# Performance work log

Measured on AMD Instinct MI355X. Metric: run time of the kernel, lower is better.

Reference implementation:

```python
import jax, jax.numpy as jnp
import numpy as np

NEG_SLOPE = 0.2  # PyG GATConv default leaky_relu negative_slope


def gat_conv(x, edge_index, W, att_src, att_dst, bias, heads, out_ch):
    """PyG GATConv (add_self_loops=False, concat=True, dropout disabled)."""
    N = x.shape[0]
    src, dst = edge_index[0], edge_index[1]
    h = (x @ W).reshape(N, heads, out_ch)               # [N,H,C]
    a_src = jnp.einsum('nhc,hc->nh', h, att_src)        # [N,H]
    a_dst = jnp.einsum('nhc,hc->nh', h, att_dst)        # [N,H]
    e = jax.nn.leaky_relu(a_src[src] + a_dst[dst], NEG_SLOPE)  # [E,H]
    # segment softmax over edges grouped by destination node
    e_max = jax.ops.segment_max(e, dst, num_segments=N)  # [N,H]
    e_exp = jnp.exp(e - e_max[dst])
    denom = jax.ops.segment_sum(e_exp, dst, num_segments=N)
    alpha = e_exp / (denom[dst] + 1e-16)                 # [E,H]
    msg = h[src] * alpha[:, :, None]                     # [E,H,C]
    out = jax.ops.segment_sum(msg, dst, num_segments=N)  # [N,H,C]
    return out.reshape(N, heads * out_ch) + bias


def setup_inputs() -> dict:
    key = jax.random.key(0)
    ks = jax.random.split(key, 10)
    N, E, F_IN, H, C1, OUT = 50000, 1600000, 256, 8, 8, 64
    s = 0.1
    return {
        'x': jax.random.normal(ks[0], (N, F_IN), jnp.float32),
        'edge_index': jax.random.randint(ks[1], (2, E), 0, N, jnp.int64),
        'W1': jax.random.normal(ks[2], (F_IN, H * C1), jnp.float32) * s,
        'att_src1': jax.random.normal(ks[3], (H, C1), jnp.float32) * s,
        'att_dst1': jax.random.normal(ks[4], (H, C1), jnp.float32) * s,
        'bias1': jax.random.normal(ks[5], (H * C1,), jnp.float32) * s,
        'W2': jax.random.normal(ks[6], (H * C1, OUT), jnp.float32) * s,
        'att_src2': jax.random.normal(ks[7], (1, OUT), jnp.float32) * s,
        'att_dst2': jax.random.normal(ks[8], (1, OUT), jnp.float32) * s,
        'bias2': jax.random.normal(ks[9], (OUT,), jnp.float32) * s,
    }


def reference(x, edge_index, W1, att_src1, att_dst1, bias1, W2, att_src2, att_dst2, bias2):
    # GAT.forward, eval mode with disable_dropout=True (no dropout, no loss)
    h = gat_conv(x, edge_index, W1, att_src1, att_dst1, bias1, heads=8, out_ch=8)
    h = jax.nn.elu(h)
    h = gat_conv(h, edge_index, W2, att_src2, att_dst2, bias2, heads=1, out_ch=64)
    return jax.nn.log_softmax(h, axis=1)
```

## Files before the change

kernel.cpp:

```cpp
#include <hip/hip_runtime.h>
#include <math.h>

#define LRELU 0.2f
#define BSH 7
#define BSZ (1 << BSH)
#define CH 8192
#define ECH 2048
#define GB 10

typedef __attribute__((ext_vector_type(8))) short bf16x8;
typedef __attribute__((ext_vector_type(4))) float f32x4;

static __device__ __forceinline__ float bf2f(unsigned int u16) {
    union { unsigned int i; float f; } c; c.i = u16 << 16; return c.f;
}
static __device__ __forceinline__ unsigned short f2bf(float f) {
    union { float f; unsigned int i; } c; c.f = f;
    unsigned int x = c.i;
    return (unsigned short)((x + 0x7fffu + ((x >> 16) & 1u)) >> 16);
}


__global__ __launch_bounds__(256) void k_prep(const int* __restrict__ dst, int E,
                                              int NB, int* __restrict__ bcnt,
                                              const float* __restrict__ W1,
                                              const float* __restrict__ W2,
                                              const float* __restrict__ as2in,
                                              const float* __restrict__ ad2in,
                                              unsigned short* __restrict__ Wt1,
                                              unsigned short* __restrict__ Wt2,
                                              unsigned short* __restrict__ h1b,
                                              unsigned short* __restrict__ gb,
                                              float* __restrict__ w2s,
                                              float* __restrict__ w2d,
                                              int* __restrict__ boff,
                                              int* __restrict__ bcur,
                                              int N, int nchunk) {
    __shared__ int cnt[512];
    __shared__ int lastFlag;
    int t = threadIdx.x;
    if ((int)blockIdx.x < nchunk) {
        for (int b = t; b < 512; b += 256) cnt[b] = 0;
        __syncthreads();
        int e0 = blockIdx.x * CH;
        int e1 = e0 + CH; if (e1 > E) e1 = E;
        for (int i = e0 + t; i < e1; i += 256) atomicAdd(&cnt[dst[i] >> BSH], 1);
        __syncthreads();
        for (int b = t; b < NB; b += 256) {
            int c = cnt[b];
            if (c) atomicAdd(&bcnt[b], c);
        }
        __syncthreads();
        if (t == 0) {
            __threadfence();
            lastFlag = (atomicAdd(&bcnt[NB], 1) == nchunk - 1);
        }
        __syncthreads();
        if (lastFlag && t < 64) {
            int lane = t;
            int run = 0;
            for (int base = 0; base < NB; base += 64) {
                int v = (base + lane < NB) ? bcnt[base + lane] : 0;
                int inc = v;
#pragma unroll
                for (int off = 1; off < 64; off <<= 1) {
                    int q = __shfl_up(inc, off, 64);
                    if (lane >= off) inc += q;
                }
                if (base + lane < NB) {
                    int e = run + inc - v;
                    boff[base + lane] = e;
                    bcur[base + lane] = e;
                }
                run += __shfl(inc, 63, 64);
            }
            if (lane == 0) boff[NB] = run;
        }
        return;
    }
    int idx = ((int)blockIdx.x - nchunk) * 256 + t;
    if (idx < 16384) {
        int n = idx >> 8, k = idx & 255;
        Wt1[idx] = f2bf(W1[k * 64 + n]);
    } else if (idx < 16384 + 4096) {
        int j = idx - 16384;
        int n = j >> 6, k = j & 63;
        Wt2[j] = f2bf(W2[k * 64 + n]);
    } else if (idx >= 20480 && idx < 20544) {
        h1b[(size_t)N * 64 + (idx - 20480)] = 0;
    } else if (idx >= 20544 && idx < 20608) {
        gb[(size_t)N * 64 + (idx - 20544)] = 0;
    } else if (idx >= 20608 && idx < 20672) {
        int c = idx - 20608;
        float s = 0.f;
#pragma unroll
        for (int n = 0; n < 64; ++n) s += W2[c * 64 + n] * as2in[n];
        w2s[c] = s;
    } else if (idx >= 20672 && idx < 20736) {
        int c = idx - 20672;
        float s = 0.f;
#pragma unroll
        for (int n = 0; n < 64; ++n) s += W2[c * 64 + n] * ad2in[n];
        w2d[c] = s;
    }
}


__global__ __launch_bounds__(256) void k_binscat1(const int* __restrict__ src,
                                                  const int* __restrict__ dst,
                                                  int E, int NB,
                                                  int* __restrict__ bcur,
                                                  unsigned* __restrict__ pairs) {
    __shared__ int cnt[512];
    __shared__ int lds_d[CH];
    int t = threadIdx.x;
    int e0 = blockIdx.x * CH;
    int e1 = e0 + CH; if (e1 > E) e1 = E;
    int n = e1 - e0;
    for (int b = t; b < 512; b += 256) cnt[b] = 0;
    __syncthreads();
    for (int i = t; i < n; i += 256) {
        int d = dst[e0 + i];
        lds_d[i] = d;
        atomicAdd(&cnt[d >> BSH], 1);
    }
    __syncthreads();
    for (int b = t; b < NB; b += 256) {
        int c = cnt[b];
        cnt[b] = c ? atomicAdd(&bcur[b], c) : 0;
    }
    __syncthreads();
    for (int i = t; i < n; i += 256) {
        int d = lds_d[i];
        int p = atomicAdd(&cnt[d >> BSH], 1);
        pairs[p] = ((unsigned)src[e0 + i] << BSH) | (unsigned)(d & (BSZ - 1));
    }
}

__global__ __launch_bounds__(256) void k_bucket(const int* __restrict__ boff,
                                                const unsigned* __restrict__ pairs,
                                                int N, int* __restrict__ rowptr,
                                                int* __restrict__ col) {
    __shared__ int cnt[BSZ];
    __shared__ int cur[BSZ];
    int t = threadIdx.x;
    int b = blockIdx.x;
    int dlo = b << BSH;
    int dhi = dlo + BSZ; if (dhi > N) dhi = N;
    int nd = dhi - dlo;
    int jb = boff[b], je = boff[b + 1];
    if (t < BSZ) cnt[t] = 0;
    __syncthreads();
    for (int j = jb + t; j < je; j += 256) atomicAdd(&cnt[pairs[j] & (BSZ - 1)], 1);
    __syncthreads();
    if (t < 64) {
        int v0 = cnt[t], v1 = cnt[64 + t];
        int i0 = v0;
#pragma unroll
        for (int off = 1; off < 64; off <<= 1) {
            int q = __shfl_up(i0, off, 64);
            if (t >= off) i0 += q;
        }
        int tot0 = __shfl(i0, 63, 64);
        int i1 = v1;
#pragma unroll
        for (int off = 1; off < 64; off <<= 1) {
            int q = __shfl_up(i1, off, 64);
            if (t >= off) i1 += q;
        }
        int e0x = jb + i0 - v0;
        int e1x = jb + tot0 + i1 - v1;
        cur[t] = e0x;
        cur[64 + t] = e1x;
        if (t < nd) rowptr[dlo + t] = e0x;
        if (64 + t < nd) rowptr[dlo + 64 + t] = e1x;
        if (t == 0 && dhi == N) rowptr[N] = je;
    }
    __syncthreads();
    for (int j = jb + t; j < je; j += 256) {
        unsigned pk = pairs[j];
        int p = atomicAdd(&cur[pk & (BSZ - 1)], 1);
        col[p] = (int)(pk >> BSH);
    }
}

__global__ __launch_bounds__(256) void k_gemm1m(const float* __restrict__ X,
                                                const unsigned short* __restrict__ Wt,
                                                const float* __restrict__ attd,
                                                int N, unsigned short* __restrict__ Hb,
                                                float* __restrict__ adst) {
    __shared__ short Xl[64 * 256];
    int t = threadIdx.x, l = t & 63, w = t >> 6;
    int rblk = blockIdx.x * 64;

    int half = l >> 5;
    int c8 = (l & 31) * 8;
#pragma unroll
    for (int i = 0; i < 8; ++i) {
        int rl = w * 16 + i * 2 + half;
        int row = rblk + rl;
        float4 x0 = {0.f, 0.f, 0.f, 0.f}, x1 = {0.f, 0.f, 0.f, 0.f};
        if (row < N) {
            x0 = *reinterpret_cast<const float4*>(X + (size_t)row * 256 + c8);
            x1 = *reinterpret_cast<const float4*>(X + (size_t)row * 256 + c8 + 4);
        }
        bf16x8 p;
        p[0] = (short)f2bf(x0.x); p[1] = (short)f2bf(x0.y);
        p[2] = (short)f2bf(x0.z); p[3] = (short)f2bf(x0.w);
        p[4] = (short)f2bf(x1.x); p[5] = (short)f2bf(x1.y);
        p[6] = (short)f2bf(x1.z); p[7] = (short)f2bf(x1.w);
        int g = (l & 31) ^ (rl & 7);
        *reinterpret_cast<bf16x8*>(&Xl[rl * 256 + g * 8]) = p;
    }

    int m = l & 15, quad = l >> 4;
    int rl = w * 16 + m;
    f32x4 acc0 = {0.f, 0.f, 0.f, 0.f}, acc1 = acc0, acc2 = acc0, acc3 = acc0;
#pragma unroll
    for (int tt = 0; tt < 8; ++tt) {
        int g = (tt * 4 + quad) ^ (m & 7);
        bf16x8 a = *reinterpret_cast<const bf16x8*>(&Xl[rl * 256 + g * 8]);
        int kk = tt * 32 + quad * 8;
        bf16x8 b0 = *reinterpret_cast<const bf16x8*>(&Wt[(0 * 16 + m) * 256 + kk]);
        bf16x8 b1 = *reinterpret_cast<const bf16x8*>(&Wt[(1 * 16 + m) * 256 + kk]);
        bf16x8 b2 = *reinterpret_cast<const bf16x8*>(&Wt[(2 * 16 + m) * 256 + kk]);
        bf16x8 b3 = *reinterpret_cast<const bf16x8*>(&Wt[(3 * 16 + m) * 256 + kk]);
        acc0 = __builtin_amdgcn_mfma_f32_16x16x32_bf16(a, b0, acc0, 0, 0, 0);
        acc1 = __builtin_amdgcn_mfma_f32_16x16x32_bf16(a, b1, acc1, 0, 0, 0);
        acc2 = __builtin_amdgcn_mfma_f32_16x16x32_bf16(a, b2, acc2, 0, 0, 0);
        acc3 = __builtin_amdgcn_mfma_f32_16x16x32_bf16(a, b3, acc3, 0, 0, 0);
    }

    int r0 = rblk + w * 16;
    f32x4 accs[4] = {acc0, acc1, acc2, acc3};
#pragma unroll
    for (int nt = 0; nt < 4; ++nt) {
        int cn = nt * 16 + m;
        float av_d = attd[cn];
#pragma unroll
        for (int r = 0; r < 4; ++r) {
            int row = r0 + quad * 4 + r;
            float hv = accs[nt][r];
            if (row < N) Hb[(size_t)row * 64 + cn] = f2bf(hv);
            float vd = hv * av_d;
            vd += __shfl_xor(vd, 1, 64); vd += __shfl_xor(vd, 2, 64); vd += __shfl_xor(vd, 4, 64);
            if ((m & 7) == 0 && row < N) {
                adst[row * 8 + (cn >> 3)] = vd;
            }
        }
    }
}


__global__ __launch_bounds__(256) void k_gather1f(const int* __restrict__ rowptr,
                                                  const int* __restrict__ col,
                                                  const uint4* __restrict__ Hb8,
                                                  const float* __restrict__ adst,
                                                  const float* __restrict__ attS,
                                                  const float* __restrict__ bias,
                                                  const unsigned short* __restrict__ Wt2,
                                                  const float* __restrict__ w2d,
                                                  int N,
                                                  unsigned short* __restrict__ Gb,
                                                  float* __restrict__ ad2) {
    __shared__ int colS[ECH];
    __shared__ short h2l[32 * 64];
    int t = threadIdx.x;
    int gid = t >> 3, sub = t & 7;
    int d0 = blockIdx.x * 32;
    int dend = d0 + 32; if (dend > N) dend = N;
    int d = d0 + gid;
    int dok = (d < dend);
    int dc = dok ? d : d0;
    int jb = rowptr[dc];
    int je = rowptr[dc + 1];
    if (!dok) { jb = 0; je = 0; }
    float adv = dok ? adst[dc * 8 + sub] : 0.f;
    float aS[8];
#pragma unroll
    for (int c = 0; c < 8; ++c) aS[c] = attS[sub * 8 + c];
    int ebeg = rowptr[d0];
    int eend = rowptr[dend];

    float acc[8] = {0.f, 0.f, 0.f, 0.f, 0.f, 0.f, 0.f, 0.f};
    float denom = 0.f;
    for (int cb = ebeg; cb < eend; cb += ECH) {
        int ce = cb + ECH; if (ce > eend) ce = eend;
        int n = ce - cb;
        __syncthreads();
        for (int i = t; i < n; i += 256) colS[i] = col[cb + i];
        __syncthreads();
        int lo = (jb > cb) ? jb : cb;
        int hi = (je < ce) ? je : ce;
        for (int u = lo; u < hi; u += GB) {
            uint4 hv8[GB];
#pragma unroll
            for (int q = 0; q < GB; ++q) {
                int uu = u + q;
                int s = (uu < hi) ? colS[uu - cb] : N;
                hv8[q] = Hb8[(size_t)s * 8 + sub];
            }
            __builtin_amdgcn_sched_barrier(0);
#pragma unroll
            for (int q = 0; q < GB; ++q) {
                uint4 hv = hv8[q];
                float f0 = bf2f(hv.x & 0xffffu), f1 = bf2f(hv.x >> 16);
                float f2 = bf2f(hv.y & 0xffffu), f3 = bf2f(hv.y >> 16);
                float f4 = bf2f(hv.z & 0xffffu), f5 = bf2f(hv.z >> 16);
                float f6 = bf2f(hv.w & 0xffffu), f7 = bf2f(hv.w >> 16);
                float ps = f0 * aS[0];
                ps = fmaf(f1, aS[1], ps); ps = fmaf(f2, aS[2], ps);
                ps = fmaf(f3, aS[3], ps); ps = fmaf(f4, aS[4], ps);
                ps = fmaf(f5, aS[5], ps); ps = fmaf(f6, aS[6], ps);
                ps = fmaf(f7, aS[7], ps);
                float e = ps + adv;
                e = (e > 0.f) ? e : LRELU * e;
                float wgt = ((u + q) < hi) ? __expf(e) : 0.f;
                denom += wgt;
                acc[0] = fmaf(wgt, f0, acc[0]); acc[1] = fmaf(wgt, f1, acc[1]);
                acc[2] = fmaf(wgt, f2, acc[2]); acc[3] = fmaf(wgt, f3, acc[3]);
                acc[4] = fmaf(wgt, f4, acc[4]); acc[5] = fmaf(wgt, f5, acc[5]);
                acc[6] = fmaf(wgt, f6, acc[6]); acc[7] = fmaf(wgt, f7, acc[7]);
            }
        }
    }

    float invd = 1.f / (denom + 1e-16f);
    float v[8];
#pragma unroll
    for (int c = 0; c < 8; ++c) {
        float x = fmaf(acc[c], invd, bias[sub * 8 + c]);
        v[c] = (x > 0.f) ? x : expm1f(x);
    }
    float vd = 0.f;
#pragma unroll
    for (int c = 0; c < 8; ++c) vd = fmaf(v[c], w2d[sub * 8 + c], vd);
    vd += __shfl_xor(vd, 1, 64); vd += __shfl_xor(vd, 2, 64); vd += __shfl_xor(vd, 4, 64);
    if (dok && sub == 0) ad2[d] = vd;

    bf16x8 p;
#pragma unroll
    for (int c = 0; c < 8; ++c) p[c] = (short)f2bf(v[c]);
    *reinterpret_cast<bf16x8*>(&h2l[gid * 64 + (sub ^ (gid & 7)) * 8]) = p;
    __syncthreads();

    int l = t & 63, w = t >> 6;
    int m = l & 15, quad = l >> 4;
    int mt = w & 1;
    int ntb = (w >> 1) * 2;
    int r = mt * 16 + m;
    f32x4 g0 = {0.f, 0.f, 0.f, 0.f}, g1 = g0;
#pragma unroll
    for (int tt = 0; tt < 2; ++tt) {
        bf16x8 a = *reinterpret_cast<const bf16x8*>(
            &h2l[r * 64 + ((tt * 4 + quad) ^ (r & 7)) * 8]);
        int kk = tt * 32 + quad * 8;
        bf16x8 b0 = *reinterpret_cast<const bf16x8*>(&Wt2[((ntb + 0) * 16 + m) * 64 + kk]);
        bf16x8 b1 = *reinterpret_cast<const bf16x8*>(&Wt2[((ntb + 1) * 16 + m) * 64 + kk]);
        g0 = __builtin_amdgcn_mfma_f32_16x16x32_bf16(a, b0, g0, 0, 0, 0);
        g1 = __builtin_amdgcn_mfma_f32_16x16x32_bf16(a, b1, g1, 0, 0, 0);
    }
    f32x4 gs[2] = {g0, g1};
#pragma unroll
    for (int nt = 0; nt < 2; ++nt) {
        int cn = (ntb + nt) * 16 + m;
#pragma unroll
        for (int rr = 0; rr < 4; ++rr) {
            int dr = d0 + mt * 16 + quad * 4 + rr;
            if (dr < N) Gb[(size_t)dr * 64 + cn] = f2bf(gs[nt][rr]);
        }
    }
}


__global__ __launch_bounds__(256) void k_gather2(const int* __restrict__ rowptr,
                                                 const int* __restrict__ col,
                                                 const uint4* __restrict__ Gb8,
                                                 const float* __restrict__ adst,
                                                 const float* __restrict__ w2s,
                                                 const float* __restrict__ bias,
                                                 int N,
                                                 float* __restrict__ out) {
    __shared__ int colS[ECH];
    int t = threadIdx.x;
    int gid = t >> 3, sub = t & 7;
    int d0 = blockIdx.x * 32;
    int dend = d0 + 32; if (dend > N) dend = N;
    int d = d0 + gid;
    int dok = (d < dend);
    int dc = dok ? d : d0;
    int jb = rowptr[dc];
    int je = rowptr[dc + 1];
    if (!dok) { jb = 0; je = 0; }
    float adv = dok ? adst[dc] : 0.f;
    float wS[8];
#pragma unroll
    for (int c = 0; c < 8; ++c) wS[c] = w2s[sub * 8 + c];
    int ebeg = rowptr[d0];
    int eend = rowptr[dend];

    float acc[8] = {0.f, 0.f, 0.f, 0.f, 0.f, 0.f, 0.f, 0.f};
    float denom = 0.f;
    for (int cb = ebeg; cb < eend; cb += ECH) {
        int ce = cb + ECH; if (ce > eend) ce = eend;
        int n = ce - cb;
        __syncthreads();
        for (int i = t; i < n; i += 256) colS[i] = col[cb + i];
        __syncthreads();
        int lo = (jb > cb) ? jb : cb;
        int hi = (je < ce) ? je : ce;
        for (int u = lo; u < hi; u += GB) {
            uint4 hv8[GB];
#pragma unroll
            for (int q = 0; q < GB; ++q) {
                int uu = u + q;
                int s = (uu < hi) ? colS[uu - cb] : N;
                hv8[q] = Gb8[(size_t)s * 8 + sub];
            }
            __builtin_amdgcn_sched_barrier(0);
#pragma unroll
            for (int q = 0; q < GB; ++q) {
                uint4 hv = hv8[q];
                float f0 = bf2f(hv.x & 0xffffu), f1 = bf2f(hv.x >> 16);
                float f2 = bf2f(hv.y & 0xffffu), f3 = bf2f(hv.y >> 16);
                float f4 = bf2f(hv.z & 0xffffu), f5 = bf2f(hv.z >> 16);
                float f6 = bf2f(hv.w & 0xffffu), f7 = bf2f(hv.w >> 16);
                float ps = f0 * wS[0];
                ps = fmaf(f1, wS[1], ps); ps = fmaf(f2, wS[2], ps);
                ps = fmaf(f3, wS[3], ps); ps = fmaf(f4, wS[4], ps);
                ps = fmaf(f5, wS[5], ps); ps = fmaf(f6, wS[6], ps);
                ps = fmaf(f7, wS[7], ps);
                ps += __shfl_xor(ps, 1, 64);
                ps += __shfl_xor(ps, 2, 64);
                ps += __shfl_xor(ps, 4, 64);
                float e = ps + adv;
                e = (e > 0.f) ? e : LRELU * e;
                float wgt = ((u + q) < hi) ? __expf(e) : 0.f;
                denom += wgt;
                acc[0] = fmaf(wgt, f0, acc[0]); acc[1] = fmaf(wgt, f1, acc[1]);
                acc[2] = fmaf(wgt, f2, acc[2]); acc[3] = fmaf(wgt, f3, acc[3]);
                acc[4] = fmaf(wgt, f4, acc[4]); acc[5] = fmaf(wgt, f5, acc[5]);
                acc[6] = fmaf(wgt, f6, acc[6]); acc[7] = fmaf(wgt, f7, acc[7]);
            }
        }
    }
    float invd = 1.f / (denom + 1e-16f);
    float v[8];
#pragma unroll
    for (int c = 0; c < 8; ++c) v[c] = fmaf(acc[c], invd, bias[sub * 8 + c]);
    float m = v[0];
#pragma unroll
    for (int c = 1; c < 8; ++c) m = fmaxf(m, v[c]);
    m = fmaxf(m, __shfl_xor(m, 1, 64));
    m = fmaxf(m, __shfl_xor(m, 2, 64));
    m = fmaxf(m, __shfl_xor(m, 4, 64));
    float se = 0.f;
#pragma unroll
    for (int c = 0; c < 8; ++c) se += __expf(v[c] - m);
    se += __shfl_xor(se, 1, 64);
    se += __shfl_xor(se, 2, 64);
    se += __shfl_xor(se, 4, 64);
    float ls = m + __logf(se);
    if (dok) {
        float4 o0, o1;
        o0.x = v[0] - ls; o0.y = v[1] - ls; o0.z = v[2] - ls; o0.w = v[3] - ls;
        o1.x = v[4] - ls; o1.y = v[5] - ls; o1.z = v[6] - ls; o1.w = v[7] - ls;
        *reinterpret_cast<float4*>(&out[(size_t)d * 64 + sub * 8]) = o0;
        *reinterpret_cast<float4*>(&out[(size_t)d * 64 + sub * 8 + 4]) = o1;
    }
}


extern "C" void kernel_launch(void* const* d_in, const int* in_sizes, int n_in,
                              void* d_out, int out_size, void* d_ws, size_t ws_size,
                              hipStream_t stream) {
    const float* x   = (const float*)d_in[0];
    const int*   ei  = (const int*)d_in[1];
    const float* W1  = (const float*)d_in[2];
    const float* as1 = (const float*)d_in[3];
    const float* ad1 = (const float*)d_in[4];
    const float* b1  = (const float*)d_in[5];
    const float* W2  = (const float*)d_in[6];
    const float* as2 = (const float*)d_in[7];
    const float* ad2 = (const float*)d_in[8];
    const float* b2  = (const float*)d_in[9];
    float* out = (float*)d_out;

    const int N = in_sizes[0] / 256;
    const int E = in_sizes[1] / 2;
    const int* src = ei;
    const int* dst = ei + E;
    const int NB = (N + BSZ - 1) >> BSH;
    const int nchunk = (E + CH - 1) / CH;

    char* ws = (char*)d_ws;
    size_t off = 0;
    auto alloc = [&](size_t bytes) -> void* {
        void* p = ws + off;
        off = (off + bytes + 255) & ~(size_t)255;
        return p;
    };
    int*      bcnt   = (int*)alloc((size_t)(NB + 1) * 4);
    int*      boff   = (int*)alloc((size_t)(NB + 1) * 4);
    int*      bcur   = (int*)alloc((size_t)NB * 4);
    int*      rowptr = (int*)alloc((size_t)(N + 1) * 4);
    int*      col    = (int*)alloc((size_t)E * 4);
    unsigned* pairs  = (unsigned*)alloc((size_t)E * 4);
    unsigned short* wt1 = (unsigned short*)alloc(64 * 256 * 2);
    unsigned short* wt2 = (unsigned short*)alloc(64 * 64 * 2);
    unsigned short* h1b = (unsigned short*)alloc((size_t)(N + 1) * 64 * 2);
    float* a_d1   = (float*)alloc((size_t)N * 8 * 4);
    unsigned short* gb  = (unsigned short*)alloc((size_t)(N + 1) * 64 * 2);
    float* a_d2   = (float*)alloc((size_t)N * 4);
    float* w2s    = (float*)alloc(64 * 4);
    float* w2d    = (float*)alloc(64 * 4);
    (void)ws_size; (void)n_in; (void)out_size;

    hipMemsetAsync(bcnt, 0, (size_t)(NB + 1) * 4, stream);
    k_prep<<<nchunk + 82, 256, 0, stream>>>(dst, E, NB, bcnt, W1, W2, as2, ad2,
                                            wt1, wt2, h1b, gb, w2s, w2d,
                                            boff, bcur, N, nchunk);

    k_binscat1<<<nchunk, 256, 0, stream>>>(src, dst, E, NB, bcur, pairs);

    int gblk = (N + 63) / 64;
    k_gemm1m<<<gblk, 256, 0, stream>>>(x, wt1, ad1, N, h1b, a_d1);

    k_bucket<<<NB, 256, 0, stream>>>(boff, pairs, N, rowptr, col);

    int gather_blocks = (N + 31) / 32;
    k_gather1f<<<gather_blocks, 256, 0, stream>>>(rowptr, col, (const uint4*)h1b,
                                                  a_d1, as1, b1, wt2, w2d,
                                                  N, gb, a_d2);

    k_gather2<<<gather_blocks, 256, 0, stream>>>(rowptr, col, (const uint4*)gb,
                                                 a_d2, w2s, b2, N, out);
}
```

Measured before the change: 252.7 us.

## Double-buffer neighbor gathers and use packed f32x2 math in GAT aggregation

Both edge-aggregation kernels now use two register buffers for gathered bf16 feature rows, so the next group's loads are issued while the current group is computed. The loop trip count is made uniform across the wavefront with a max reduction over shuffles, which keeps the cross-lane shuffles in layer 2 safe. The bf16 unpack, dot product and accumulation are rewritten with 2-wide float vectors so the compiler can emit packed FMA instructions. The group size drops from 10 to 6 to limit register pressure from the two buffers, at the cost of extra masked iterations and gathers of the padding row for destinations with short edge lists.

New measurement: 260.8 us. 1.03x slower.

```diff
diff --git a/kernel.cpp b/kernel.cpp
--- a/kernel.cpp
+++ b/kernel.cpp
@@ -6,10 +6,11 @@
 #define BSZ (1 << BSH)
 #define CH 8192
 #define ECH 2048
-#define GB 10
+#define GB 6
 
 typedef __attribute__((ext_vector_type(8))) short bf16x8;
 typedef __attribute__((ext_vector_type(4))) float f32x4;
+typedef __attribute__((ext_vector_type(2))) float f32x2;
 
 static __device__ __forceinline__ float bf2f(unsigned int u16) {
     union { unsigned int i; float f; } c; c.i = u16 << 16; return c.f;
@@ -18,6 +19,11 @@
     union { float f; unsigned int i; } c; c.f = f;
     unsigned int x = c.i;
     return (unsigned short)((x + 0x7fffu + ((x >> 16) & 1u)) >> 16);
+}
+static __device__ __forceinline__ f32x2 unpk(unsigned int u) {
+    union { unsigned int i; float f; } lo, hi;
+    lo.i = u << 16; hi.i = u & 0xffff0000u;
+    f32x2 r; r[0] = lo.f; r[1] = hi.f; return r;
 }
 
 
@@ -276,14 +282,43 @@
     int je = rowptr[dc + 1];
     if (!dok) { jb = 0; je = 0; }
     float adv = dok ? adst[dc * 8 + sub] : 0.f;
-    float aS[8];
-#pragma unroll
-    for (int c = 0; c < 8; ++c) aS[c] = attS[sub * 8 + c];
+    f32x2 aS2[4];
+#pragma unroll
+    for (int j = 0; j < 4; ++j) {
+        aS2[j][0] = attS[sub * 8 + 2 * j];
+        aS2[j][1] = attS[sub * 8 + 2 * j + 1];
+    }
     int ebeg = rowptr[d0];
     int eend = rowptr[dend];
 
-    float acc[8] = {0.f, 0.f, 0.f, 0.f, 0.f, 0.f, 0.f, 0.f};
+    f32x2 ac2[4] = {{0.f, 0.f}, {0.f, 0.f}, {0.f, 0.f}, {0.f, 0.f}};
     float denom = 0.f;
+
+#define LOAD1(hv, ub)                                                       \
+    _Pragma("unroll")                                                       \
+    for (int q = 0; q < GB; ++q) {                                          \
+        int uu = (ub) + q;                                                  \
+        int s = (uu < hi) ? colS[uu - cb] : N;                              \
+        hv[q] = Hb8[(size_t)s * 8 + sub];                                   \
+    }                                                                       \
+    __builtin_amdgcn_sched_barrier(0);
+
+#define COMP1(hv, ub)                                                       \
+    _Pragma("unroll")                                                       \
+    for (int q = 0; q < GB; ++q) {                                          \
+        uint4 h = hv[q];                                                    \
+        f32x2 p0 = unpk(h.x), p1 = unpk(h.y), p2 = unpk(h.z), p3 = unpk(h.w); \
+        f32x2 ps2 = p0 * aS2[0];                                            \
+        ps2 += p1 * aS2[1]; ps2 += p2 * aS2[2]; ps2 += p3 * aS2[3];         \
+        float ps = ps2[0] + ps2[1] + adv;                                   \
+        float e = (ps > 0.f) ? ps : LRELU * ps;                             \
+        float wgt = (((ub) + q) < hi) ? __expf(e) : 0.f;                    \
+        denom += wgt;                                                       \
+        f32x2 w2 = {wgt, wgt};                                              \
+        ac2[0] += w2 * p0; ac2[1] += w2 * p1;                               \
+        ac2[2] += w2 * p2; ac2[3] += w2 * p3;                               \
+    }
+
     for (int cb = ebeg; cb < eend; cb += ECH) {
         int ce = cb + ECH; if (ce > eend) ce = eend;
         int n = ce - cb;
@@ -292,44 +327,34 @@
         __syncthreads();
         int lo = (jb > cb) ? jb : cb;
         int hi = (je < ce) ? je : ce;
-        for (int u = lo; u < hi; u += GB) {
-            uint4 hv8[GB];
-#pragma unroll
-            for (int q = 0; q < GB; ++q) {
-                int uu = u + q;
-                int s = (uu < hi) ? colS[uu - cb] : N;
-                hv8[q] = Hb8[(size_t)s * 8 + sub];
-            }
-            __builtin_amdgcn_sched_barrier(0);
-#pragma unroll
-            for (int q = 0; q < GB; ++q) {
-                uint4 hv = hv8[q];
-                float f0 = bf2f(hv.x & 0xffffu), f1 = bf2f(hv.x >> 16);
-                float f2 = bf2f(hv.y & 0xffffu), f3 = bf2f(hv.y >> 16);
-                float f4 = bf2f(hv.z & 0xffffu), f5 = bf2f(hv.z >> 16);
-                float f6 = bf2f(hv.w & 0xffffu), f7 = bf2f(hv.w >> 16);
-                float ps = f0 * aS[0];
-                ps = fmaf(f1, aS[1], ps); ps = fmaf(f2, aS[2], ps);
-                ps = fmaf(f3, aS[3], ps); ps = fmaf(f4, aS[4], ps);
-                ps = fmaf(f5, aS[5], ps); ps = fmaf(f6, aS[6], ps);
-                ps = fmaf(f7, aS[7], ps);
-                float e = ps + adv;
-                e = (e > 0.f) ? e : LRELU * e;
-                float wgt = ((u + q) < hi) ? __expf(e) : 0.f;
-                denom += wgt;
-                acc[0] = fmaf(wgt, f0, acc[0]); acc[1] = fmaf(wgt, f1, acc[1]);
-                acc[2] = fmaf(wgt, f2, acc[2]); acc[3] = fmaf(wgt, f3, acc[3]);
-                acc[4] = fmaf(wgt, f4, acc[4]); acc[5] = fmaf(wgt, f5, acc[5]);
-                acc[6] = fmaf(wgt, f6, acc[6]); acc[7] = fmaf(wgt, f7, acc[7]);
-            }
-        }
-    }
+        int len = hi - lo; if (len < 0) len = 0;
+        int nit = (len + GB - 1) / GB;
+        int nmax = nit;
+        nmax = max(nmax, __shfl_xor(nmax, 8, 64));
+        nmax = max(nmax, __shfl_xor(nmax, 16, 64));
+        nmax = max(nmax, __shfl_xor(nmax, 32, 64));
+        int n2 = (nmax + 1) >> 1;
+
+        uint4 hvA[GB], hvB[GB];
+        int uA = lo, uB = lo + GB;
+        LOAD1(hvA, uA)
+        for (int p = 0; p < n2; ++p) {
+            LOAD1(hvB, uB)
+            COMP1(hvA, uA)
+            uA = uB + GB;
+            LOAD1(hvA, uA)
+            COMP1(hvB, uB)
+            uB = uA + GB;
+        }
+    }
+#undef LOAD1
+#undef COMP1
 
     float invd = 1.f / (denom + 1e-16f);
     float v[8];
 #pragma unroll
     for (int c = 0; c < 8; ++c) {
-        float x = fmaf(acc[c], invd, bias[sub * 8 + c]);
+        float x = fmaf(ac2[c >> 1][c & 1], invd, bias[sub * 8 + c]);
         v[c] = (x > 0.f) ? x : expm1f(x);
     }
     float vd = 0.f;
@@ -393,14 +418,47 @@
     int je = rowptr[dc + 1];
     if (!dok) { jb = 0; je = 0; }
     float adv = dok ? adst[dc] : 0.f;
-    float wS[8];
-#pragma unroll
-    for (int c = 0; c < 8; ++c) wS[c] = w2s[sub * 8 + c];
+    f32x2 wS2[4];
+#pragma unroll
+    for (int j = 0; j < 4; ++j) {
+        wS2[j][0] = w2s[sub * 8 + 2 * j];
+        wS2[j][1] = w2s[sub * 8 + 2 * j + 1];
+    }
     int ebeg = rowptr[d0];
     int eend = rowptr[dend];
 
-    float acc[8] = {0.f, 0.f, 0.f, 0.f, 0.f, 0.f, 0.f, 0.f};
+    f32x2 ac2[4] = {{0.f, 0.f}, {0.f, 0.f}, {0.f, 0.f}, {0.f, 0.f}};
     float denom = 0.f;
+
+#define LOAD2(hv, ub)                                                       \
+    _Pragma("unroll")                                                       \
+    for (int q = 0; q < GB; ++q) {                                          \
+        int uu = (ub) + q;                                                  \
+        int s = (uu < hi) ? colS[uu - cb] : N;                              \
+        hv[q] = Gb8[(size_t)s * 8 + sub];                                   \
+    }                                                                       \
+    __builtin_amdgcn_sched_barrier(0);
+
+#define COMP2(hv, ub)                                                       \
+    _Pragma("unroll")                                                       \
+    for (int q = 0; q < GB; ++q) {                                          \
+        uint4 h = hv[q];                                                    \
+        f32x2 p0 = unpk(h.x), p1 = unpk(h.y), p2 = unpk(h.z), p3 = unpk(h.w); \
+        f32x2 ps2 = p0 * wS2[0];                                            \
+        ps2 += p1 * wS2[1]; ps2 += p2 * wS2[2]; ps2 += p3 * wS2[3];         \
+        float ps = ps2[0] + ps2[1];                                         \
+        ps += __shfl_xor(ps, 1, 64);                                        \
+        ps += __shfl_xor(ps, 2, 64);                                        \
+        ps += __shfl_xor(ps, 4, 64);                                        \
+        float e = ps + adv;                                                 \
+        e = (e > 0.f) ? e : LRELU * e;                                      \
+        float wgt = (((ub) + q) < hi) ? __expf(e) : 0.f;                    \
+        denom += wgt;                                                       \
+        f32x2 w2 = {wgt, wgt};                                              \
+        ac2[0] += w2 * p0; ac2[1] += w2 * p1;                               \
+        ac2[2] += w2 * p2; ac2[3] += w2 * p3;                               \
+    }
+
     for (int cb = ebeg; cb < eend; cb += ECH) {
         int ce = cb + ECH; if (ce > eend) ce = eend;
         int n = ce - cb;
@@ -409,45 +467,33 @@
         __syncthreads();
         int lo = (jb > cb) ? jb : cb;
         int hi = (je < ce) ? je : ce;
-        for (int u = lo; u < hi; u += GB) {
-            uint4 hv8[GB];
-#pragma unroll
-            for (int q = 0; q < GB; ++q) {
-                int uu = u + q;
-                int s = (uu < hi) ? colS[uu - cb] : N;
-                hv8[q] = Gb8[(size_t)s * 8 + sub];
-            }
-            __builtin_amdgcn_sched_barrier(0);
-#pragma unroll
-            for (int q = 0; q < GB; ++q) {
-                uint4 hv = hv8[q];
-                float f0 = bf2f(hv.x & 0xffffu), f1 = bf2f(hv.x >> 16);
-                float f2 = bf2f(hv.y & 0xffffu), f3 = bf2f(hv.y >> 16);
-                float f4 = bf2f(hv.z & 0xffffu), f5 = bf2f(hv.z >> 16);
-                float f6 = bf2f(hv.w & 0xffffu), f7 = bf2f(hv.w >> 16);
-                float ps = f0 * wS[0];
-                ps = fmaf(f1, wS[1], ps); ps = fmaf(f2, wS[2], ps);
-                ps = fmaf(f3, wS[3], ps); ps = fmaf(f4, wS[4], ps);
-                ps = fmaf(f5, wS[5], ps); ps = fmaf(f6, wS[6], ps);
-                ps = fmaf(f7, wS[7], ps);
-                ps += __shfl_xor(ps, 1, 64);
-                ps += __shfl_xor(ps, 2, 64);
-                ps += __shfl_xor(ps, 4, 64);
-                float e = ps + adv;
-                e = (e > 0.f) ? e : LRELU * e;
-                float wgt = ((u + q) < hi) ? __expf(e) : 0.f;
-                denom += wgt;
-                acc[0] = fmaf(wgt, f0, acc[0]); acc[1] = fmaf(wgt, f1, acc[1]);
-                acc[2] = fmaf(wgt, f2, acc[2]); acc[3] = fmaf(wgt, f3, acc[3]);
-                acc[4] = fmaf(wgt, f4, acc[4]); acc[5] = fmaf(wgt, f5, acc[5]);
-                acc[6] = fmaf(wgt, f6, acc[6]); acc[7] = fmaf(wgt, f7, acc[7]);
-            }
-        }
-    }
+        int len = hi - lo; if (len < 0) len = 0;
+        int nit = (len + GB - 1) / GB;
+        int nmax = nit;
+        nmax = max(nmax, __shfl_xor(nmax, 8, 64));
+        nmax = max(nmax, __shfl_xor(nmax, 16, 64));
+        nmax = max(nmax, __shfl_xor(nmax, 32, 64));
+        int n2 = (nmax + 1) >> 1;
+
+        uint4 hvA[GB], hvB[GB];
+        int uA = lo, uB = lo + GB;
+        LOAD2(hvA, uA)
+        for (int p = 0; p < n2; ++p) {
+            LOAD2(hvB, uB)
+            COMP2(hvA, uA)
+            uA = uB + GB;
+            LOAD2(hvA, uA)
+            COMP2(hvB, uB)
+            uB = uA + GB;
+        }
+    }
+#undef LOAD2
+#undef COMP2
+
     float invd = 1.f / (denom + 1e-16f);
     float v[8];
 #pragma unroll
-    for (int c = 0; c < 8; ++c) v[c] = fmaf(acc[c], invd, bias[sub * 8 + c]);
+    for (int c = 0; c < 8; ++c) v[c] = fmaf(ac2[c >> 1][c & 1], invd, bias[sub * 8 + c]);
     float m = v[0];
 #pragma unroll
     for (int c = 1; c < 8; ++c) m = fmaxf(m, v[c]);
```
